# Performance work log

Hardware: AMD Instinct MI355X
Metric: run time of the kernel (lower is better)

## Reference

```python
import jax, jax.numpy as jnp
import numpy as np

EPS = 1e-4
SLOPE = 0.01
NFFT = 512
HOP = 256
CH_IN = 8
CH_H = 64
FREQ = NFFT // 2 + 1
LEN = 48000
BATCH = 2


def hann(n):
    return (0.5 - 0.5 * jnp.cos(2.0 * np.pi * jnp.arange(n) / n)).astype(jnp.float32)


def stft(x):
    # x: (B, C, L) -> (B, 2, C, F, T)  (torch.stft: center=True, reflect pad, hann window)
    pad = NFFT // 2
    xp = jnp.pad(x, ((0, 0), (0, 0), (pad, pad)), mode='reflect')
    T = 1 + x.shape[-1] // HOP
    idx = jnp.arange(T)[:, None] * HOP + jnp.arange(NFFT)[None, :]
    frames = xp[..., idx] * hann(NFFT)            # (B, C, T, NFFT)
    sp = jnp.fft.rfft(frames, axis=-1)            # (B, C, T, F)
    sp = jnp.swapaxes(sp, -1, -2)                 # (B, C, F, T)
    return jnp.stack([sp.real, sp.imag], axis=1).astype(jnp.float32)


def istft(re, im, length):
    # re, im: (B, C, F, T) -> (B, C, length) via windowed overlap-add
    sp = jnp.swapaxes(re + 1j * im, -1, -2)       # (B, C, T, F)
    win = hann(NFFT)
    frames = jnp.fft.irfft(sp, n=NFFT, axis=-1) * win
    pad = NFFT // 2
    total = length + 2 * pad
    T = frames.shape[-2]
    idx = jnp.arange(T)[:, None] * HOP + jnp.arange(NFFT)[None, :]
    out = jnp.zeros(frames.shape[:-2] + (total,), frames.dtype).at[..., idx].add(frames)
    wsum = jnp.zeros((total,), frames.dtype).at[idx].add(jnp.broadcast_to(win ** 2, (T, NFFT)))
    return (out / jnp.maximum(wsum, 1e-11))[..., pad:pad + length]


def conv2d(x, w, b, padT=0):
    y = jax.lax.conv_general_dilated(x, w, (1, 1), ((0, 0), (padT, padT)),
                                     dimension_numbers=('NCHW', 'OIHW', 'NCHW'))
    return y + b[None, :, None, None]


def cconv(x, w, b, padT=0):
    # complex conv on x: (B,2,C,F,T); w: (2,O,C,kf,kt) = [W_real, W_imag]; b: (2,O)
    r = conv2d(x[:, 0], w[0], b[0], padT) - conv2d(x[:, 1], w[1], b[1], padT)
    i = conv2d(x[:, 1], w[0], b[0], padT) + conv2d(x[:, 0], w[1], b[1], padT)
    return jnp.stack([r, i], axis=1)


def modExp(x, m=5.0):
    em = float(np.exp(m))
    return jnp.where(x > m, (x - m) * em + em, jnp.exp(jnp.minimum(x, m)))


def cExp(t):
    e = modExp(t[:, 0]) - 1.0
    return jnp.stack([e * jnp.cos(t[:, 1] - 1.0), e * jnp.sin(t[:, 1] - 1.0)], axis=1)


def snap(x):
    x = jnp.where((x >= 0) & (x < EPS), EPS, x)
    return jnp.where((x < 0) & (x > -EPS), -EPS, x)


def cLog(t):
    re = snap(t[:, 0])
    im = snap(t[:, 1])
    real = jnp.log(jnp.sqrt(im ** 2 + re ** 2 + EPS ** 2) + 1.0)
    imag = jnp.arctan(im / re)
    return jnp.stack([real, imag], axis=1)


def cMul(a, b):
    r = a[:, 0] * b[:, 0] - a[:, 1] * b[:, 1]
    i = a[:, 0] * b[:, 1] + a[:, 1] * b[:, 0]
    return jnp.stack([r, i], axis=1)


def trelu(t, tr, b):
    nr = t[:, 0] * tr[0, 0] + t[:, 1] * tr[0, 1] + b[0]
    ni = t[:, 0] * tr[1, 0] + t[:, 1] * tr[1, 1] + b[1]
    return jnp.stack([jax.nn.leaky_relu(nr, SLOPE), jax.nn.leaky_relu(ni, SLOPE)], axis=1)


def tgate(t, tr, b):
    gr = jax.nn.sigmoid(t[:, 0] * tr[0, 0] + t[:, 1] * tr[0, 1] + b[0])
    gi = jax.nn.sigmoid(t[:, 0] * tr[1, 0] + t[:, 1] * tr[1, 1] + b[1])
    return gr * gi + (1.0 - gr) * (1.0 - gi)


def perm(t):
    return jnp.transpose(t, (0, 1, 3, 2, 4))


def lrelu(x):
    return jax.nn.leaky_relu(x, SLOPE)


def forward(mix, fs_w, fs_b, fr_w, fr_b, c1r_w, c1r_b, c1i_w, c1i_b, c1_w, c1_b,
            c2r_w, c2r_b, c2i_w, c2i_b, c2_w, c2_b, a1_t, a1_b, a2_t, a2_b,
            c3r_w, c3r_b, c3i_w, c3i_b, c3_w, c3_b, c4r_w, c4r_b, c4i_w, c4i_b,
            c4_w, c4_b, a3_t, a3_b, a4_t, a4_b, f1_w, f1_b, f2_w, f2_b,
            cw_w, cw_b, fg_t, fg_b):
    ts = perm(cconv(perm(stft(mix)), fs_w, fs_b))      # (B,2,C,F,T)
    # ---- branch 1 ----
    tl = cLog(ts)
    tl = jnp.stack([conv2d(tl[:, 0], c1r_w, c1r_b), conv2d(tl[:, 1], c1r_w, c1r_b)], 1)
    tl = jnp.stack([conv2d(lrelu(tl[:, 0]), c1i_w, c1i_b), conv2d(tl[:, 1], c1i_w, c1i_b)], 1)
    tl = trelu(cExp(tl), a1_t, a1_b)
    t = cconv(tl, c1_w, c1_b)
    tl = cLog(t)
    tl = jnp.stack([conv2d(tl[:, 0], c2r_w, c2r_b, 7), conv2d(tl[:, 1], c2r_w, c2r_b, 7)], 1)[..., :-7]
    tl = jnp.stack([conv2d(lrelu(tl[:, 0]), c2i_w, c2i_b, 7), conv2d(tl[:, 1], c2i_w, c2i_b, 7)], 1)[..., :-7]
    tl = cExp(tl)
    tl1 = tl
    tc = cconv(ts, c2_w, c2_b, 7)[..., :-7]
    t = trelu(cMul(tl, tc), a2_t, a2_b)
    t = cconv(t, f1_w, f1_b)
    td1 = jnp.sum(ts - t, axis=2, keepdims=True) / ts.shape[2]
    # ---- branch 2 ----
    tl = cLog(ts)
    tl = jnp.stack([conv2d(tl[:, 0], c3r_w, c3r_b), conv2d(tl[:, 1], c3r_w, c3r_b)], 1)
    tl = jnp.stack([conv2d(lrelu(tl[:, 0]), c3i_w, c3i_b), conv2d(tl[:, 1], c3i_w, c3i_b)], 1)
    tl = trelu(cExp(tl), a3_t, a3_b)
    t = cconv(tl, c3_w, c3_b)
    tl = cLog(t)
    tl = jnp.stack([conv2d(tl[:, 0], c4r_w, c4r_b, 7), conv2d(tl[:, 1], c4r_w, c4r_b, 7)], 1)[..., :-7]
    tl = jnp.stack([conv2d(lrelu(tl[:, 0]), c4i_w, c4i_b, 7), conv2d(tl[:, 1], c4i_w, c4i_b, 7)], 1)[..., :-7]
    tl = cExp(tl)
    tc = cconv(ts, c4_w, c4_b, 7)[..., :-7]
    t = trelu(cMul(tl, tc), a4_t, a4_b)
    td2 = cconv(t, f2_w, f2_b)                         # (B,2,1,F,T)
    # ---- fuse ----
    f = cconv(jnp.concatenate([tl1, tl], axis=2), cw_w, cw_b)
    f = tgate(f, fg_t, fg_b)[:, None]                  # (B,1,1,F,T)
    td = td1 * f + td2 * (1.0 - f)
    t = perm(cconv(perm(td), fr_w, fr_b))
    return istft(t[:, 0], t[:, 1], LEN)                # (B,1,LEN)


def setup_inputs() -> dict:
    ks = iter(jax.random.split(jax.random.key(0), 64))
    def rn(shape, s=0.05):
        return s * jax.random.normal(next(ks), shape, jnp.float32)
    F, C, H = FREQ, CH_IN, CH_H
    inp = {
        'mix': jax.random.normal(next(ks), (BATCH, C, LEN), jnp.float32),
        'fs_w': rn((2, F, F, 1, 1)), 'fs_b': rn((2, F), 0.01),
        'fr_w': rn((2, F, F, 1, 1)), 'fr_b': rn((2, F), 0.01),
        'c1r_w': rn((H, C, 1, 1)), 'c1r_b': rn((H,), 0.01),
        'c1i_w': rn((H, H, 1, 1)), 'c1i_b': rn((H,), 0.01),
        'c1_w': rn((2, H, H, 1, 1)), 'c1_b': rn((2, H), 0.01),
        'c2r_w': rn((H, H, 1, 8)), 'c2r_b': rn((H,), 0.01),
        'c2i_w': rn((H, H, 1, 8)), 'c2i_b': rn((H,), 0.01),
        'c2_w': rn((2, H, C, 1, 8)), 'c2_b': rn((2, H), 0.01),
        'a1_t': rn((2, 2, H, F, 1), 0.5), 'a1_b': rn((2, H, F, 1), 0.5),
        'a2_t': rn((2, 2, H, F, 1), 0.5), 'a2_b': rn((2, H, F, 1), 0.5),
        'c3r_w': rn((H, C, 1, 1)), 'c3r_b': rn((H,), 0.01),
        'c3i_w': rn((H, H, 1, 1)), 'c3i_b': rn((H,), 0.01),
        'c3_w': rn((2, H, H, 1, 1)), 'c3_b': rn((2, H), 0.01),
        'c4r_w': rn((H, H, 1, 8)), 'c4r_b': rn((H,), 0.01),
        'c4i_w': rn((H, H, 1, 8)), 'c4i_b': rn((H,), 0.01),
        'c4_w': rn((2, H, C, 1, 8)), 'c4_b': rn((2, H), 0.01),
        'a3_t': rn((2, 2, H, F, 1), 0.5), 'a3_b': rn((2, H, F, 1), 0.5),
        'a4_t': rn((2, 2, H, F, 1), 0.5), 'a4_b': rn((2, H, F, 1), 0.5),
        'f1_w': rn((2, C, H, 1, 1)), 'f1_b': rn((2, C), 0.01),
        'f2_w': rn((2, 1, H, 1, 1)), 'f2_b': rn((2, 1), 0.01),
        'cw_w': rn((2, 1, 2 * H, 1, 1)), 'cw_b': rn((2, 1), 0.01),
        'fg_t': rn((2, 2, 1, F, 1), 0.5), 'fg_b': rn((2, 1, F, 1), 0.5),
    }
    return inp


def reference(mix, fs_w, fs_b, fr_w, fr_b, c1r_w, c1r_b, c1i_w, c1i_b, c1_w, c1_b,
              c2r_w, c2r_b, c2i_w, c2i_b, c2_w, c2_b, a1_t, a1_b, a2_t, a2_b,
              c3r_w, c3r_b, c3i_w, c3i_b, c3_w, c3_b, c4r_w, c4r_b, c4i_w, c4i_b,
              c4_w, c4_b, a3_t, a3_b, a4_t, a4_b, f1_w, f1_b, f2_w, f2_b,
              cw_w, cw_b, fg_t, fg_b):
    return forward(mix, fs_w, fs_b, fr_w, fr_b, c1r_w, c1r_b, c1i_w, c1i_b, c1_w, c1_b,
                   c2r_w, c2r_b, c2i_w, c2i_b, c2_w, c2_b, a1_t, a1_b, a2_t, a2_b,
                   c3r_w, c3r_b, c3i_w, c3i_b, c3_w, c3_b, c4r_w, c4r_b, c4i_w, c4i_b,
                   c4_w, c4_b, a3_t, a3_b, a4_t, a4_b, f1_w, f1_b, f2_w, f2_b,
                   cw_w, cw_b, fg_t, fg_b)
```

## Files before the change

kernel.cpp:

```cpp
#include <hip/hip_runtime.h>
#include <math.h>

#define DEV __device__ __forceinline__

constexpr int B_   = 2;
constexpr int C_IN = 8;
constexpr int H_   = 64;
constexpr int F_   = 257;
constexpr int T_   = 188;
constexpr int TW   = 96;
constexpr int NFFT = 512;
constexpr int HOP  = 256;
constexpr int LEN  = 48000;
constexpr int PADL = 256;
constexpr int FT   = F_ * T_;
constexpr float EPSV  = 1e-4f;
constexpr float SLOPEV = 0.01f;
constexpr float PI2 = 6.283185307179586f;

typedef __attribute__((ext_vector_type(8))) short short8;
typedef __attribute__((ext_vector_type(4))) short short4v;
typedef __attribute__((ext_vector_type(4))) float float4v;

DEV float lrelu_f(float x) { return x > 0.f ? x : SLOPEV * x; }
DEV float snap_f(float x) {
  if (x >= 0.f && x < EPSV) return EPSV;
  if (x < 0.f && x > -EPSV) return -EPSV;
  return x;
}
DEV float fast_atan(float z) {
  float az = fabsf(z);
  float u = az > 1.f ? __builtin_amdgcn_rcpf(az) : az;
  float u2 = u * u;
  float p = -0.01172120f;
  p = p * u2 + 0.05265332f;
  p = p * u2 - 0.11643287f;
  p = p * u2 + 0.19354346f;
  p = p * u2 - 0.33262347f;
  p = p * u2 + 0.99997726f;
  float r = p * u;
  if (az > 1.f) r = 1.5707963267948966f - r;
  return z < 0.f ? -r : r;
}
DEV float modexp_f(float x) {
  const float em = 148.4131591025766f;
  return x > 5.f ? (x - 5.f) * em + em : __expf(x);
}
DEV void cexp_f(float tr, float ti, float& er, float& ei) {
  float e = modexp_f(tr) - 1.f;
  float a = ti - 1.f;
  er = e * __cosf(a); ei = e * __sinf(a);
}
DEV float sigmoid_f(float x) { return 1.f / (1.f + __expf(-x)); }

DEV short f2bf(float x) {
  unsigned u = __float_as_uint(x);
  unsigned r = (u + 0x7fffu + ((u >> 16) & 1u)) >> 16;
  return (short)r;
}
DEV float bf2f(short h) {
  return __uint_as_float(((unsigned)(unsigned short)h) << 16);
}
DEV unsigned pack_hl(float v) {
  short hi = f2bf(v);
  short lo = f2bf(v - bf2f(hi));
  return ((unsigned)(unsigned short)hi << 16) | (unsigned)(unsigned short)lo;
}

__global__ void k_mixsplit(const float* __restrict__ x, short* __restrict__ hi,
                           short* __restrict__ lo) {
  int i = blockIdx.x * 256 + threadIdx.x;
  if (i >= B_ * C_IN * LEN / 4) return;
  float4v v = *(const float4v*)(x + (size_t)i * 4);
  short4v h, l;
  #pragma unroll
  for (int j = 0; j < 4; ++j) {
    h[j] = f2bf(v[j]);
    l[j] = f2bf(v[j] - bf2f(h[j]));
  }
  *(short4v*)(hi + (size_t)i * 4) = h;
  *(short4v*)(lo + (size_t)i * 4) = l;
}

__global__ __launch_bounds__(256) void k_mixdft(const float* __restrict__ W,
                                                short* __restrict__ wpk) {
  constexpr int MT = 33;
  __shared__ float wr_s[F_], wi_s[F_];
  int m = blockIdx.x;
  int k = blockIdx.y * 256 + threadIdx.x;
  int po = m >= F_;
  int fo = m - po * F_;
  if (m < 2 * F_) {
    for (int i = threadIdx.x; i < F_; i += 256) {
      wr_s[i] = W[fo * F_ + i];
      wi_s[i] = W[F_ * F_ + fo * F_ + i];
    }
  }
  __syncthreads();
  float val = 0.f;
  if (m < 2 * F_) {
    float sd, cd;
    sincosf((PI2 / NFFT) * k, &sd, &cd);
    float cs = 1.f, sn = 0.f;
    float ar = 0.f, ai = 0.f;
    for (int fi = 0; fi < F_; ++fi) {
      float wrv = wr_s[fi], wiv = wi_s[fi];
      ar += wrv * cs + wiv * sn;
      ai += wiv * cs - wrv * sn;
      float t2 = cs * cd - sn * sd;
      sn = sn * cd + cs * sd;
      cs = t2;
    }
    float win = 0.5f - 0.5f * cd;
    val = (po ? ai : ar) * win;
  }
  int mtg = m >> 4;
  int lane2 = ((k >> 3) & 3) * 16 + (m & 15);
  int s = k >> 5;
  int j = k & 7;
  short hi = f2bf(val);
  short lo = f2bf(val - bf2f(hi));
  wpk[(((0 * 16 + s) * MT + mtg) * 64 + lane2) * 8 + j] = hi;
  wpk[(((16 + s) * MT + mtg) * 64 + lane2) * 8 + j] = lo;
}

constexpr int TWS = 48;
__global__ __launch_bounds__(256) void k_stftmix(
    const short* __restrict__ mhi, const short* __restrict__ mlo,
    const short* __restrict__ wpk, const float* __restrict__ bias,
    float* __restrict__ Y) {
  constexpr int PITCH = 136;
  constexpr int MT = 33;
  __shared__ short xs_hi[TWS * PITCH];
  __shared__ short xs_lo[TWS * PITCH];
  int mg = blockIdx.x;
  int bc = blockIdx.y;
  int b = bc >> 3, c = bc & 7;
  int t0 = blockIdx.z * TWS;
  int tid = threadIdx.x;
  int lane = tid & 63;
  int wv = __builtin_amdgcn_readfirstlane(tid >> 6);
  int mtg = mg * 4 + wv;
  int q = lane >> 4;
  int n = lane & 15;

  const short* mh_ = mhi + (size_t)(b * C_IN + c) * LEN;
  const short* ml_ = mlo + (size_t)(b * C_IN + c) * LEN;

  float4v acc[3];
  #pragma unroll
  for (int nt = 0; nt < 3; ++nt) acc[nt] = (float4v)(0.f);

  const short8* wp = (const short8*)wpk;
  for (int round = 0; round < 4; ++round) {
    if (round) __syncthreads();
    for (int i = tid; i < TWS * 16; i += 256) {
      int tl = i >> 4, u = i & 15;
      int kk0 = u * 8;
      int t = t0 + tl;
      int g0 = t * HOP + round * 128 + kk0 - PADL;
      short8 h, l;
      if (t < T_ && g0 >= 0 && g0 + 7 < LEN) {
        h = *(const short8*)(mh_ + g0);
        l = *(const short8*)(ml_ + g0);
      } else {
        #pragma unroll
        for (int j = 0; j < 8; ++j) {
          short hv = 0, lv = 0;
          if (t < T_) {
            int g = g0 + j;
            if (g < 0) g = -g;
            if (g >= LEN) g = 2 * LEN - 2 - g;
            hv = mh_[g]; lv = ml_[g];
          }
          h[j] = hv; l[j] = lv;
        }
      }
      *(short8*)&xs_hi[tl * PITCH + kk0] = h;
      *(short8*)&xs_lo[tl * PITCH + kk0] = l;
    }
    __syncthreads();
    #pragma unroll
    for (int s2 = 0; s2 < 4; ++s2) {
      int s = round * 4 + s2;
      short8 Ah, Al;
      if (mtg < MT) {
        Ah = wp[((0 * 16 + s) * MT + mtg) * 64 + lane];
        Al = wp[((16 + s) * MT + mtg) * 64 + lane];
      }
      short8 Bh[3], Bl[3];
      #pragma unroll
      for (int nt = 0; nt < 3; ++nt) {
        int off = (nt * 16 + n) * PITCH + s2 * 32 + q * 8;
        Bh[nt] = *(const short8*)&xs_hi[off];
        Bl[nt] = *(const short8*)&xs_lo[off];
      }
      if (mtg < MT) {
        #pragma unroll
        for (int nt = 0; nt < 3; ++nt) {
          acc[nt] = __builtin_amdgcn_mfma_f32_16x16x32_bf16(Ah, Bh[nt], acc[nt], 0, 0, 0);
          acc[nt] = __builtin_amdgcn_mfma_f32_16x16x32_bf16(Ah, Bl[nt], acc[nt], 0, 0, 0);
          acc[nt] = __builtin_amdgcn_mfma_f32_16x16x32_bf16(Al, Bh[nt], acc[nt], 0, 0, 0);
        }
      }
    }
  }

  if (mtg < MT) {
    #pragma unroll
    for (int nt = 0; nt < 3; ++nt) {
      int t = t0 + nt * 16 + n;
      if (t >= T_) continue;
      #pragma unroll
      for (int r = 0; r < 4; ++r) {
        int m = mtg * 16 + q * 4 + r;
        if (m >= 2 * F_) continue;
        int po = m >= F_;
        int fo = m - po * F_;
        float badd = po ? bias[fo] + bias[F_ + fo] : bias[fo] - bias[F_ + fo];
        Y[((size_t)((b * 2 + po) * C_IN + c)) * FT + fo * T_ + t] = acc[nt][r] + badd;
      }
    }
  }
}

template<int CH>
__global__ void k_fmix(const float* __restrict__ X, const float* __restrict__ W,
                       const float* __restrict__ bias, float* __restrict__ Y) {
  int fo = blockIdx.x;
  int bc = blockIdx.y; int c = bc % CH; int b = bc / CH;
  int t = threadIdx.x;
  if (t >= T_) return;
  const float* wr = W + fo * F_;
  const float* wi = W + F_ * F_ + fo * F_;
  const float* xr = X + ((b * 2 + 0) * CH + c) * FT + t;
  const float* xi = X + ((b * 2 + 1) * CH + c) * FT + t;
  float ar = 0.f, ai = 0.f;
  for (int fi = 0; fi < F_; ++fi) {
    float wrv = wr[fi], wiv = wi[fi];
    float xrv = xr[fi * T_], xiv = xi[fi * T_];
    ar += wrv * xrv - wiv * xiv;
    ai += wrv * xiv + wiv * xrv;
  }
  float br = bias[fo], bi = bias[F_ + fo];
  Y[((b * 2 + 0) * CH + c) * FT + fo * T_ + t] = ar + br - bi;
  Y[((b * 2 + 1) * CH + c) * FT + fo * T_ + t] = ai + br + bi;
}

template<int CIN, int K>
DEV void repack_real_body(const float* __restrict__ W, short* __restrict__ wpk, int i) {
  constexpr int CC = (CIN >= 32) ? (CIN / 32) : 1;
  constexpr int NSTEP = (CIN * K + 31) / 32;
  int total = 2 * NSTEP * 4 * 64 * 8;
  if (i >= total) return;
  int j = i & 7;
  int lane = (i >> 3) & 63;
  int mt = (i >> 9) & 3;
  int s = (i >> 11) % NSTEP;
  int split = i / (NSTEP * 2048);
  int q = lane >> 4;
  int m = mt * 16 + (lane & 15);
  int tap = s / CC;
  int c = (s % CC) * 32 + q * 8 + j;
  float w = 0.f;
  if (c < CIN && tap < K) w = W[(m * CIN + c) * K + tap];
  short hi = f2bf(w);
  wpk[i] = split ? f2bf(w - bf2f(hi)) : hi;
}

template<int CIN2, int COUT2, int K>
DEV void repack_cplx_body(const float* __restrict__ W, short* __restrict__ wpk, int i) {
  constexpr int CIN = CIN2 / 2, COUT = COUT2 / 2;
  constexpr int NSTEP = CIN2 * K / 32;
  constexpr int MT = (COUT2 + 15) / 16;
  int total = 2 * NSTEP * MT * 64 * 8;
  if (i >= total) return;
  int j = i & 7;
  int lane = (i >> 3) & 63;
  int idx = i >> 9;
  int mt = idx % MT; idx /= MT;
  int s = idx % NSTEP;
  int split = idx / NSTEP;
  int q = lane >> 4;
  int m = mt * 16 + (lane & 15);
  int tap, pi, ci;
  if constexpr (CIN2 == 128) {
    tap = 0;
    int cs = s * 32 + q * 8 + j;
    int half = cs / 64, r = cs % 64;
    ci = half * 32 + r / 2;
    pi = r & 1;
  } else {
    tap = s * 2 + (q >> 1);
    int cs = (q & 1) * 8 + j;
    pi = cs / CIN;
    ci = cs % CIN;
  }
  float w = 0.f;
  if (m < COUT2) {
    int po = m / COUT, ho = m % COUT;
    float wr = W[((0 * COUT + ho) * CIN + ci) * K + tap];
    float wi = W[((1 * COUT + ho) * CIN + ci) * K + tap];
    w = (po == pi) ? wr : (po == 0 ? -wi : wi);
  }
  short hi = f2bf(w);
  wpk[i] = split ? f2bf(w - bf2f(hi)) : hi;
}

__global__ __launch_bounds__(256) void k_repack_all(
    const float* c1r_w, const float* c1i_w, const float* c2r_w, const float* c2i_w,
    const float* c3r_w, const float* c3i_w, const float* c4r_w, const float* c4i_w,
    const float* c1_w, const float* c2_w, const float* c3_w, const float* c4_w,
    const float* f1_w, const float* f2_w,
    short* o0, short* o1, short* o2, short* o3, short* o4, short* o5, short* o6,
    short* o7, short* o8, short* o9, short* o10, short* o11, short* o12, short* o13) {
  int i = blockIdx.x * 256 + threadIdx.x;
  switch (blockIdx.y) {
    case 0:  repack_real_body<C_IN, 1>(c1r_w, o0, i); break;
    case 1:  repack_real_body<H_,   1>(c1i_w, o1, i); break;
    case 2:  repack_real_body<H_,   8>(c2r_w, o2, i); break;
    case 3:  repack_real_body<H_,   8>(c2i_w, o3, i); break;
    case 4:  repack_real_body<C_IN, 1>(c3r_w, o4, i); break;
    case 5:  repack_real_body<H_,   1>(c3i_w, o5, i); break;
    case 6:  repack_real_body<H_,   8>(c4r_w, o6, i); break;
    case 7:  repack_real_body<H_,   8>(c4i_w, o7, i); break;
    case 8:  repack_cplx_body<128, 128, 1>(c1_w, o8, i); break;
    case 9:  repack_cplx_body<16,  128, 8>(c2_w, o9, i); break;
    case 10: repack_cplx_body<128, 128, 1>(c3_w, o10, i); break;
    case 11: repack_cplx_body<16,  128, 8>(c4_w, o11, i); break;
    case 12: repack_cplx_body<128, 16,  1>(f1_w, o12, i); break;
    case 13: repack_cplx_body<128, 2,   1>(f2_w, o13, i); break;
  }
}

template<int CIN, int K, int PRO, int EPI>
__global__ __launch_bounds__(256) void k_conv_mfma(
    const float* __restrict__ X, const short* __restrict__ wpk,
    const float* __restrict__ bias, float* __restrict__ Y) {
  constexpr int CC = (CIN >= 32) ? (CIN / 32) : 1;
  constexpr int NSTEP = (CIN * K + 31) / 32;
  constexpr int PITCH = 72;
  constexpr int ROWS = TW + (K - 1);
  __shared__ short xs_hi[ROWS * PITCH];
  __shared__ short xs_lo[ROWS * PITCH];
  int f = blockIdx.x;
  int bp = blockIdx.y; int p = bp & 1; int b = bp >> 1;
  int t0 = blockIdx.z * TW;
  int tid = threadIdx.x;

  {
    int lo_inval = (K - 1) - t0;
    if (lo_inval < 0) lo_inval = 0;
    int hi_start = T_ - t0 + (K - 1);
    if (hi_start > ROWS) hi_start = ROWS;
    for (int i = tid; i < lo_inval * PITCH; i += 256) { xs_hi[i] = 0; xs_lo[i] = 0; }
    int nhi = (ROWS - hi_start) * PITCH;
    for (int i = tid; i < nhi; i += 256) {
      int o = hi_start * PITCH + i;
      xs_hi[o] = 0; xs_lo[o] = 0;
    }
    if (CIN < 32) {
      constexpr int BAND = 32 - ((CIN < 32) ? CIN : 32);
      for (int i = tid; i < ROWS * BAND; i += 256) {
        int rr = i / BAND, c = CIN + i % BAND;
        xs_hi[rr * PITCH + c] = 0; xs_lo[rr * PITCH + c] = 0;
      }
    }
  }
  __syncthreads();

  const float* Xr_ = X + (size_t)((b * 2 + 0) * CIN) * FT + f * T_;
  const float* Xi_ = X + (size_t)((b * 2 + 1) * CIN) * FT + f * T_;
  const float* Xp  = X + (size_t)((b * 2 + p) * CIN) * FT + f * T_;
  const unsigned* Xu = (const unsigned*)X + (size_t)((b * 2 + p) * CIN) * FT + f * T_;
  {
    constexpr int STEP_C = 256 / ROWS, STEP_R = 256 % ROWS;
    int c = tid / ROWS;
    int rr = tid - c * ROWS;
    while (c < CIN) {
      int t = t0 + rr - (K - 1);
      if (t >= 0 && t < T_) {
        short hi, lo;
        if (PRO == 3) {
          unsigned v = Xu[c * FT + t];
          hi = (short)(v >> 16);
          lo = (short)(v & 0xffffu);
        } else {
          float v;
          if (PRO == 2) {
            float re = snap_f(Xr_[c * FT + t]);
            float im = snap_f(Xi_[c * FT + t]);
            v = (p == 0) ? __logf(sqrtf(im * im + re * re + EPSV * EPSV) + 1.f)
                         : fast_atan(im / re);
          } else {
            v = Xp[c * FT + t];
            if (PRO == 1 && p == 0) v = lrelu_f(v);
          }
          hi = f2bf(v);
          lo = f2bf(v - bf2f(hi));
        }
        xs_hi[rr * PITCH + c] = hi;
        xs_lo[rr * PITCH + c] = lo;
      }
      rr += STEP_R; c += STEP_C;
      if (rr >= ROWS) { rr -= ROWS; c += 1; }
    }
  }
  __syncthreads();

  int lane = tid & 63;
  int wv = __builtin_amdgcn_readfirstlane(tid >> 6);
  int mh = wv >> 1;
  int tc = wv & 1;
  int q = lane >> 4;
  int n = lane & 15;
  int wbase = tc * 48;

  float4v acc[2][3];
  #pragma unroll
  for (int mt = 0; mt < 2; ++mt)
    #pragma unroll
    for (int nt = 0; nt < 3; ++nt) acc[mt][nt] = (float4v)(0.f);

  const short8* wp = (const short8*)wpk;
  #pragma unroll
  for (int s = 0; s < NSTEP; ++s) {
    int tap = s / CC;
    int c0 = (s % CC) * 32;
    short8 Ah[2], Al[2];
    #pragma unroll
    for (int mt = 0; mt < 2; ++mt) {
      int mtg = mh * 2 + mt;
      Ah[mt] = wp[((0 * NSTEP + s) * 4 + mtg) * 64 + lane];
      Al[mt] = wp[((1 * NSTEP + s) * 4 + mtg) * 64 + lane];
    }
    short8 Bh[3], Bl[3];
    #pragma unroll
    for (int nt = 0; nt < 3; ++nt) {
      int off = (wbase + nt * 16 + n + tap) * PITCH + c0 + q * 8;
      Bh[nt] = *(const short8*)&xs_hi[off];
      Bl[nt] = *(const short8*)&xs_lo[off];
    }
    #pragma unroll
    for (int mt = 0; mt < 2; ++mt) {
      #pragma unroll
      for (int nt = 0; nt < 3; ++nt) {
        acc[mt][nt] = __builtin_amdgcn_mfma_f32_16x16x32_bf16(Ah[mt], Bh[nt], acc[mt][nt], 0, 0, 0);
        acc[mt][nt] = __builtin_amdgcn_mfma_f32_16x16x32_bf16(Ah[mt], Bl[nt], acc[mt][nt], 0, 0, 0);
        acc[mt][nt] = __builtin_amdgcn_mfma_f32_16x16x32_bf16(Al[mt], Bh[nt], acc[mt][nt], 0, 0, 0);
      }
    }
  }

  float* Yp = Y + (size_t)((b * 2 + p) * H_) * FT + f * T_;
  unsigned* Yu = (unsigned*)Y + (size_t)((b * 2 + p) * H_) * FT + f * T_;
  #pragma unroll
  for (int nt = 0; nt < 3; ++nt) {
    int t = t0 + wbase + nt * 16 + n;
    if (t >= T_) continue;
    #pragma unroll
    for (int mt = 0; mt < 2; ++mt) {
      #pragma unroll
      for (int r = 0; r < 4; ++r) {
        int h = (mh * 2 + mt) * 16 + q * 4 + r;
        float v = acc[mt][nt][r] + bias[h];
        if (EPI == 0) {
          Yp[h * FT + t] = v;
        } else {
          if (EPI == 1 && p == 0) v = lrelu_f(v);
          Yu[h * FT + t] = pack_hl(v);
        }
      }
    }
  }
}

template<int COUT2, int PRO>
__global__ __launch_bounds__(256) void k_cconv128(
    const float* __restrict__ X0, const float* __restrict__ X1,
    const short* __restrict__ wpk,
    const float* __restrict__ at, const float* __restrict__ ab,
    const float* __restrict__ bias, float* __restrict__ Y) {
  constexpr int MT = (COUT2 + 15) / 16;
  constexpr int MTW = (MT > 4) ? 4 : MT;
  constexpr int COUT = COUT2 / 2;
  constexpr int NSTEP = 4;
  constexpr int PITCH = 72;
  __shared__ short xs_hi[TW * PITCH];
  __shared__ short xs_lo[TW * PITCH];
  __shared__ float coef[6][64];
  int f = blockIdx.x;
  int b = blockIdx.y;
  int t0 = blockIdx.z * TW;
  int tid = threadIdx.x;
  int lane = tid & 63;
  int wv = __builtin_amdgcn_readfirstlane(tid >> 6);
  int mh = wv >> 1;
  int tc = wv & 1;
  int q = lane >> 4;
  int n = lane & 15;
  int wbase = tc * 48;

  if (tid < 64) {
    int h = tid;
    coef[0][h] = at[(0 * H_ + h) * F_ + f];
    coef[1][h] = at[(1 * H_ + h) * F_ + f];
    coef[2][h] = at[(2 * H_ + h) * F_ + f];
    coef[3][h] = at[(3 * H_ + h) * F_ + f];
    coef[4][h] = ab[h * F_ + f];
    coef[5][h] = ab[(H_ + h) * F_ + f];
  }
  {
    int inval0 = T_ - t0;
    if (inval0 < 0) inval0 = 0;
    if (inval0 > TW) inval0 = TW;
    int nfill = (TW - inval0) * PITCH;
    for (int i = tid; i < nfill; i += 256) {
      int o = inval0 * PITCH + i;
      xs_hi[o] = 0; xs_lo[o] = 0;
    }
  }

  const float* b0r = X0 + (size_t)((b * 2 + 0) * H_) * FT + f * T_;
  const float* b0i = X0 + (size_t)((b * 2 + 1) * H_) * FT + f * T_;
  const float* b1r = X1 + (size_t)((b * 2 + 0) * H_) * FT + f * T_;
  const float* b1i = X1 + (size_t)((b * 2 + 1) * H_) * FT + f * T_;

  float4v acc[MTW][3];
  #pragma unroll
  for (int mt = 0; mt < MTW; ++mt)
    #pragma unroll
    for (int nt = 0; nt < 3; ++nt) acc[mt][nt] = (float4v)(0.f);

  const short8* wp = (const short8*)wpk;
  for (int half = 0; half < 2; ++half) {
    __syncthreads();
    for (int i = tid; i < 32 * TW; i += 256) {
      int hh = i / TW, tl = i % TW;
      int t = t0 + tl;
      if (t >= T_) continue;
      int h = half * 32 + hh;
      float xr = b0r[h * FT + t], xi = b0i[h * FT + t];
      float vr, vi;
      if (PRO == 1) {
        float er, ei;
        cexp_f(xr, xi, er, ei);
        vr = lrelu_f(er * coef[0][h] + ei * coef[1][h] + coef[4][h]);
        vi = lrelu_f(er * coef[2][h] + ei * coef[3][h] + coef[5][h]);
      } else {
        float yr = b1r[h * FT + t], yi = b1i[h * FT + t];
        float mr = xr * yr - xi * yi;
        float mi = xr * yi + xi * yr;
        vr = lrelu_f(mr * coef[0][h] + mi * coef[1][h] + coef[4][h]);
        vi = lrelu_f(mr * coef[2][h] + mi * coef[3][h] + coef[5][h]);
      }
      int cs0 = hh * 2, cs1 = hh * 2 + 1;
      short hr = f2bf(vr), hi2 = f2bf(vi);
      xs_hi[tl * PITCH + cs0] = hr;
      xs_lo[tl * PITCH + cs0] = f2bf(vr - bf2f(hr));
      xs_hi[tl * PITCH + cs1] = hi2;
      xs_lo[tl * PITCH + cs1] = f2bf(vi - bf2f(hi2));
    }
    __syncthreads();
    #pragma unroll
    for (int s2 = 0; s2 < 2; ++s2) {
      int s = half * 2 + s2;
      short8 Bh[3], Bl[3];
      #pragma unroll
      for (int nt = 0; nt < 3; ++nt) {
        int off = (wbase + nt * 16 + n) * PITCH + s2 * 32 + q * 8;
        Bh[nt] = *(const short8*)&xs_hi[off];
        Bl[nt] = *(const short8*)&xs_lo[off];
      }
      #pragma unroll
      for (int mt = 0; mt < MTW; ++mt) {
        int mtg = mh * 4 + mt;
        if (mtg >= MT) continue;
        short8 Ah = wp[((0 * NSTEP + s) * MT + mtg) * 64 + lane];
        short8 Al = wp[((1 * NSTEP + s) * MT + mtg) * 64 + lane];
        #pragma unroll
        for (int nt = 0; nt < 3; ++nt) {
          acc[mt][nt] = __builtin_amdgcn_mfma_f32_16x16x32_bf16(Ah, Bh[nt], acc[mt][nt], 0, 0, 0);
          acc[mt][nt] = __builtin_amdgcn_mfma_f32_16x16x32_bf16(Ah, Bl[nt], acc[mt][nt], 0, 0, 0);
          acc[mt][nt] = __builtin_amdgcn_mfma_f32_16x16x32_bf16(Al, Bh[nt], acc[mt][nt], 0, 0, 0);
        }
      }
    }
  }

  float* Yp = Y + (size_t)b * COUT2 * FT + f * T_;
  #pragma unroll
  for (int nt = 0; nt < 3; ++nt) {
    int t = t0 + wbase + nt * 16 + n;
    if (t >= T_) continue;
    #pragma unroll
    for (int mt = 0; mt < MTW; ++mt) {
      int mtg = mh * 4 + mt;
      if (mtg >= MT) continue;
      #pragma unroll
      for (int r = 0; r < 4; ++r) {
        int o2 = mtg * 16 + q * 4 + r;
        if (o2 >= COUT2) continue;
        int po = o2 / COUT, ho = o2 % COUT;
        float br = bias[ho], bi = bias[COUT + ho];
        float badd = (po == 0) ? br - bi : br + bi;
        Yp[o2 * FT + t] = acc[mt][nt][r] + badd;
      }
    }
  }
}

__global__ __launch_bounds__(256) void k_cconv16(
    const float* __restrict__ X, const short* __restrict__ wpk,
    const float* __restrict__ bias, float* __restrict__ Y) {
  constexpr int MT = 8, NSTEP = 4, PITCH = 24, ROWS = TW + 7, COUT = 64, COUT2 = 128;
  __shared__ short xs_hi[ROWS * PITCH];
  __shared__ short xs_lo[ROWS * PITCH];
  int f = blockIdx.x;
  int b = blockIdx.y;
  int t0 = blockIdx.z * TW;
  int tid = threadIdx.x;

  {
    int lo_inval = 7 - t0;
    if (lo_inval < 0) lo_inval = 0;
    int hi_start = T_ - t0 + 7;
    if (hi_start > ROWS) hi_start = ROWS;
    for (int i = tid; i < lo_inval * PITCH; i += 256) { xs_hi[i] = 0; xs_lo[i] = 0; }
    int nhi = (ROWS - hi_start) * PITCH;
    for (int i = tid; i < nhi; i += 256) {
      int o = hi_start * PITCH + i;
      xs_hi[o] = 0; xs_lo[o] = 0;
    }
  }
  __syncthreads();

  const float* Xp = X + (size_t)b * 16 * FT + f * T_;
  for (int i = tid; i < 16 * ROWS; i += 256) {
    int c = i / ROWS, rr = i % ROWS;
    int t = t0 + rr - 7;
    if (t < 0 || t >= T_) continue;
    float v = Xp[c * FT + t];
    short hi = f2bf(v);
    short lo = f2bf(v - bf2f(hi));
    xs_hi[rr * PITCH + c] = hi;
    xs_lo[rr * PITCH + c] = lo;
  }
  __syncthreads();

  int lane = tid & 63;
  int wv = __builtin_amdgcn_readfirstlane(tid >> 6);
  int mh = wv >> 1;
  int tc = wv & 1;
  int q = lane >> 4;
  int n = lane & 15;
  int wbase = tc * 48;

  float4v acc[4][3];
  #pragma unroll
  for (int mt = 0; mt < 4; ++mt)
    #pragma unroll
    for (int nt = 0; nt < 3; ++nt) acc[mt][nt] = (float4v)(0.f);

  const short8* wp = (const short8*)wpk;
  #pragma unroll
  for (int s = 0; s < NSTEP; ++s) {
    int tap = s * 2 + (q >> 1);
    int coff = (q & 1) * 8;
    short8 Bh[3], Bl[3];
    #pragma unroll
    for (int nt = 0; nt < 3; ++nt) {
      int off = (wbase + nt * 16 + n + tap) * PITCH + coff;
      Bh[nt] = *(const short8*)&xs_hi[off];
      Bl[nt] = *(const short8*)&xs_lo[off];
    }
    #pragma unroll
    for (int mt = 0; mt < 4; ++mt) {
      int mtg = mh * 4 + mt;
      short8 Ah = wp[((0 * NSTEP + s) * MT + mtg) * 64 + lane];
      short8 Al = wp[((1 * NSTEP + s) * MT + mtg) * 64 + lane];
      #pragma unroll
      for (int nt = 0; nt < 3; ++nt) {
        acc[mt][nt] = __builtin_amdgcn_mfma_f32_16x16x32_bf16(Ah, Bh[nt], acc[mt][nt], 0, 0, 0);
        acc[mt][nt] = __builtin_amdgcn_mfma_f32_16x16x32_bf16(Ah, Bl[nt], acc[mt][nt], 0, 0, 0);
        acc[mt][nt] = __builtin_amdgcn_mfma_f32_16x16x32_bf16(Al, Bh[nt], acc[mt][nt], 0, 0, 0);
      }
    }
  }

  float* Yp = Y + (size_t)b * COUT2 * FT + f * T_;
  #pragma unroll
  for (int nt = 0; nt < 3; ++nt) {
    int t = t0 + wbase + nt * 16 + n;
    if (t >= T_) continue;
    #pragma unroll
    for (int mt = 0; mt < 4; ++mt) {
      #pragma unroll
      for (int r = 0; r < 4; ++r) {
        int o2 = (mh * 4 + mt) * 16 + q * 4 + r;
        int po = o2 / COUT, ho = o2 % COUT;
        float br = bias[ho], bi = bias[COUT + ho];
        float badd = (po == 0) ? br - bi : br + bi;
        Yp[o2 * FT + t] = acc[mt][nt][r] + badd;
      }
    }
  }
}

__global__ void k_cexp_pk(const unsigned* __restrict__ X, float* __restrict__ Y) {
  int i = blockIdx.x * blockDim.x + threadIdx.x;
  if (i >= B_ * H_ * FT) return;
  int b = i / (H_ * FT);
  int r = i % (H_ * FT);
  size_t i0 = (size_t)(b * 2) * H_ * FT + r;
  size_t i1 = i0 + (size_t)H_ * FT;
  unsigned v0 = X[i0], v1 = X[i1];
  float tr = bf2f((short)(v0 >> 16)) + bf2f((short)(v0 & 0xffffu));
  float ti = bf2f((short)(v1 >> 16)) + bf2f((short)(v1 & 0xffffu));
  float er, ei;
  cexp_f(tr, ti, er, ei);
  Y[i0] = er;
  Y[i1] = ei;
}

__global__ void k_td1(const float* __restrict__ ts, const float* __restrict__ t8,
                      float* __restrict__ td1) {
  int i = blockIdx.x * blockDim.x + threadIdx.x;
  if (i >= B_ * 2 * FT) return;
  int bp = i / FT; int r = i % FT;
  const float* a = ts + bp * C_IN * FT + r;
  const float* c2 = t8 + bp * C_IN * FT + r;
  float acc = 0.f;
  #pragma unroll
  for (int c = 0; c < C_IN; ++c) acc += a[c * FT] - c2[c * FT];
  td1[i] = acc * (1.f / C_IN);
}

__global__ void k_fuse(const float* __restrict__ tl1, const float* __restrict__ tl2,
                       const float* __restrict__ td1, const float* __restrict__ td2,
                       const float* __restrict__ cw, const float* __restrict__ cwb,
                       const float* __restrict__ fgt, const float* __restrict__ fgb,
                       float* __restrict__ td) {
  int i = blockIdx.x * blockDim.x + threadIdx.x;
  if (i >= B_ * FT) return;
  int b = i / FT; int r = i % FT; int f = r / T_;
  const float* x1r = tl1 + (b * 2) * H_ * FT + r;
  const float* x1i = x1r + H_ * FT;
  const float* x2r = tl2 + (b * 2) * H_ * FT + r;
  const float* x2i = x2r + H_ * FT;
  float fr = 0.f, fi = 0.f;
  for (int c = 0; c < H_; ++c) {
    float w1r = cw[c], w2r = cw[H_ + c], w1i = cw[2 * H_ + c], w2i = cw[3 * H_ + c];
    float a1r = x1r[c * FT], a1i = x1i[c * FT];
    float a2r = x2r[c * FT], a2i = x2i[c * FT];
    fr += w1r * a1r - w1i * a1i + w2r * a2r - w2i * a2i;
    fi += w1r * a1i + w1i * a1r + w2r * a2i + w2i * a2r;
  }
  fr += cwb[0] - cwb[1];
  fi += cwb[0] + cwb[1];
  float t00 = fgt[f], t01 = fgt[F_ + f], t10 = fgt[2 * F_ + f], t11 = fgt[3 * F_ + f];
  float gr = sigmoid_f(fr * t00 + fi * t01 + fgb[f]);
  float gi = sigmoid_f(fr * t10 + fi * t11 + fgb[F_ + f]);
  float gg = gr * gi + (1.f - gr) * (1.f - gi);
  int i0 = (b * 2) * FT + r, i1 = i0 + FT;
  td[i0] = td1[i0] * gg + td2[i0] * (1.f - gg);
  td[i1] = td1[i1] * gg + td2[i1] * (1.f - gg);
}

__global__ __launch_bounds__(320) void k_iframes(const float* __restrict__ sp,
                                                 float* __restrict__ frames) {
  __shared__ float Xr[F_], Xi[F_];
  int blk = blockIdx.x;
  int t = blk % T_;
  int b = blk / T_;
  int tid = threadIdx.x;
  for (int i = tid; i < F_; i += 320) {
    Xr[i] = sp[(b * 2 + 0) * FT + i * T_ + t];
    Xi[i] = sp[(b * 2 + 1) * FT + i * T_ + t];
  }
  __syncthreads();
  int n = tid;
  if (n <= 256) {
    float sd, cd;
    sincosf((PI2 / NFFT) * n, &sd, &cd);
    float cs = cd, sn = sd;
    float ac = 0.f, as = 0.f;
    for (int f = 1; f < 256; ++f) {
      ac += Xr[f] * cs;
      as += Xi[f] * sn;
      float t2 = cs * cd - sn * sd;
      sn = sn * cd + cs * sd;
      cs = t2;
    }
    float base = Xr[0] + Xr[256] * (1.f - 2.f * (n & 1));
    float win = 0.5f - 0.5f * cd;
    float scale = win * (1.f / NFFT);
    float* fr = frames + (size_t)(b * T_ + t) * NFFT;
    fr[n] = (base + 2.f * ac - 2.f * as) * scale;
    if (n >= 1 && n <= 255)
      fr[NFFT - n] = (base + 2.f * ac + 2.f * as) * scale;
  }
}

__global__ void k_ola(const float* __restrict__ frames, float* __restrict__ out) {
  int i = blockIdx.x * blockDim.x + threadIdx.x;
  if (i >= B_ * LEN) return;
  int b = i / LEN; int j = i % LEN;
  int p = j + PADL;
  int t0 = p / HOP; int n0 = p - t0 * HOP;
  float acc = 0.f, wsum = 0.f;
  if (t0 < T_) {
    acc += frames[(b * T_ + t0) * NFFT + n0];
    float w = 0.5f - 0.5f * __cosf((PI2 / NFFT) * n0);
    wsum += w * w;
  }
  int t1 = t0 - 1, n1 = n0 + HOP;
  if (t1 >= 0 && t1 < T_) {
    acc += frames[(b * T_ + t1) * NFFT + n1];
    float w = 0.5f - 0.5f * __cosf((PI2 / NFFT) * n1);
    wsum += w * w;
  }
  out[i] = acc / fmaxf(wsum, 1e-11f);
}

extern "C" void kernel_launch(void* const* d_in, const int* in_sizes, int n_in,
                              void* d_out, int out_size, void* d_ws, size_t ws_size,
                              hipStream_t stream) {
  const float* mix   = (const float*)d_in[0];
  const float* fs_w  = (const float*)d_in[1];
  const float* fs_b  = (const float*)d_in[2];
  const float* fr_w  = (const float*)d_in[3];
  const float* fr_b  = (const float*)d_in[4];
  const float* c1r_w = (const float*)d_in[5];
  const float* c1r_b = (const float*)d_in[6];
  const float* c1i_w = (const float*)d_in[7];
  const float* c1i_b = (const float*)d_in[8];
  const float* c1_w  = (const float*)d_in[9];
  const float* c1_b  = (const float*)d_in[10];
  const float* c2r_w = (const float*)d_in[11];
  const float* c2r_b = (const float*)d_in[12];
  const float* c2i_w = (const float*)d_in[13];
  const float* c2i_b = (const float*)d_in[14];
  const float* c2_w  = (const float*)d_in[15];
  const float* c2_b  = (const float*)d_in[16];
  const float* a1_t  = (const float*)d_in[17];
  const float* a1_b  = (const float*)d_in[18];
  const float* a2_t  = (const float*)d_in[19];
  const float* a2_b  = (const float*)d_in[20];
  const float* c3r_w = (const float*)d_in[21];
  const float* c3r_b = (const float*)d_in[22];
  const float* c3i_w = (const float*)d_in[23];
  const float* c3i_b = (const float*)d_in[24];
  const float* c3_w  = (const float*)d_in[25];
  const float* c3_b  = (const float*)d_in[26];
  const float* c4r_w = (const float*)d_in[27];
  const float* c4r_b = (const float*)d_in[28];
  const float* c4i_w = (const float*)d_in[29];
  const float* c4i_b = (const float*)d_in[30];
  const float* c4_w  = (const float*)d_in[31];
  const float* c4_b  = (const float*)d_in[32];
  const float* a3_t  = (const float*)d_in[33];
  const float* a3_b  = (const float*)d_in[34];
  const float* a4_t  = (const float*)d_in[35];
  const float* a4_b  = (const float*)d_in[36];
  const float* f1_w  = (const float*)d_in[37];
  const float* f1_b  = (const float*)d_in[38];
  const float* f2_w  = (const float*)d_in[39];
  const float* f2_b  = (const float*)d_in[40];
  const float* cw_w  = (const float*)d_in[41];
  const float* cw_b  = (const float*)d_in[42];
  const float* fg_t  = (const float*)d_in[43];
  const float* fg_b  = (const float*)d_in[44];

  const size_t S8 = (size_t)B_ * 2 * C_IN * FT;
  const size_t SH = (size_t)B_ * 2 * H_ * FT;
  const size_t S1 = (size_t)B_ * 2 * FT;
  float* ws  = (float*)d_ws;
  float* ts0 = ws;
  float* ts  = ts0 + S8;
  float* A   = ts + S8;
  float* Bb  = A + SH;
  float* Cc  = Bb + SH;
  float* td1 = Cc + SH;
  float* td2 = td1 + S1;
  float* tdf = td2 + S1;
  float* tdr = tdf + S1;
  float* s8  = ts0;
  float* frames = ts0;

  short* wtail = (short*)(tdr + S1);
  constexpr int SZ_C8K1   = 2 * 1  * 4 * 64 * 8;
  constexpr int SZ_C64K1  = 2 * 2  * 4 * 64 * 8;
  constexpr int SZ_C64K8  = 2 * 16 * 4 * 64 * 8;
  constexpr int SZ_CC128  = 2 * 4  * 8 * 64 * 8;
  constexpr int SZ_CF     = 2 * 4  * 1 * 64 * 8;
  constexpr int SZ_SM     = 2 * 16 * 33 * 64 * 8;
  short* w_c1r = wtail;
  short* w_c1i = w_c1r + SZ_C8K1;
  short* w_c2r = w_c1i + SZ_C64K1;
  short* w_c2i = w_c2r + SZ_C64K8;
  short* w_c3r = w_c2i + SZ_C64K8;
  short* w_c3i = w_c3r + SZ_C8K1;
  short* w_c4r = w_c3i + SZ_C64K1;
  short* w_c4i = w_c4r + SZ_C64K8;
  short* w_cc1 = w_c4i + SZ_C64K8;
  short* w_cc2 = w_cc1 + SZ_CC128;
  short* w_cc3 = w_cc2 + SZ_CC128;
  short* w_cc4 = w_cc3 + SZ_CC128;
  short* w_cf1 = w_cc4 + SZ_CC128;
  short* w_cf2 = w_cf1 + SZ_CF;
  short* w_sm  = w_cf2 + SZ_CF;
  short* mhi   = w_sm + SZ_SM;
  short* mlo   = mhi + (size_t)B_ * C_IN * LEN;

  const int nH = B_ * H_ * FT;
  const int nP = B_ * FT;
  const dim3 rgrid(F_, B_ * 2, 2);
  const dim3 cgrid(F_, B_, 2);

  k_repack_all<<<dim3(256, 14), 256, 0, stream>>>(
      c1r_w, c1i_w, c2r_w, c2i_w, c3r_w, c3i_w, c4r_w, c4i_w,
      c1_w, c2_w, c3_w, c4_w, f1_w, f2_w,
      w_c1r, w_c1i, w_c2r, w_c2i, w_c3r, w_c3i, w_c4r, w_c4i,
      w_cc1, w_cc2, w_cc3, w_cc4, w_cf1, w_cf2);

  k_mixsplit<<<(B_ * C_IN * LEN / 4 + 255) / 256, 256, 0, stream>>>(mix, mhi, mlo);
  k_mixdft<<<dim3(528, 2), 256, 0, stream>>>(fs_w, w_sm);
  k_stftmix<<<dim3(9, 16, 4), 256, 0, stream>>>(mhi, mlo, w_sm, fs_b, ts);

  k_conv_mfma<C_IN, 1, 2, 1><<<rgrid, 256, 0, stream>>>(ts, w_c1r, c1r_b, A);
  k_conv_mfma<H_, 1, 3, 0><<<rgrid, 256, 0, stream>>>(A, w_c1i, c1i_b, Bb);
  k_cconv128<128, 1><<<cgrid, 256, 0, stream>>>(Bb, Bb, w_cc1, a1_t, a1_b, c1_b, A);
  k_conv_mfma<H_, 8, 2, 1><<<rgrid, 256, 0, stream>>>(A, w_c2r, c2r_b, Bb);
  k_conv_mfma<H_, 8, 3, 2><<<rgrid, 256, 0, stream>>>(Bb, w_c2i, c2i_b, A);
  k_cexp_pk<<<(nH + 255) / 256, 256, 0, stream>>>((const unsigned*)A, Bb);
  k_cconv16<<<cgrid, 256, 0, stream>>>(ts, w_cc2, c2_b, A);
  k_cconv128<16, 2><<<cgrid, 256, 0, stream>>>(Bb, A, w_cf1, a2_t, a2_b, f1_b, s8);
  k_td1<<<(B_ * 2 * FT + 255) / 256, 256, 0, stream>>>(ts, s8, td1);

  k_conv_mfma<C_IN, 1, 2, 1><<<rgrid, 256, 0, stream>>>(ts, w_c3r, c3r_b, A);
  k_conv_mfma<H_, 1, 3, 0><<<rgrid, 256, 0, stream>>>(A, w_c3i, c3i_b, Cc);
  k_cconv128<128, 1><<<cgrid, 256, 0, stream>>>(Cc, Cc, w_cc3, a3_t, a3_b, c3_b, A);
  k_conv_mfma<H_, 8, 2, 1><<<rgrid, 256, 0, stream>>>(A, w_c4r, c4r_b, Cc);
  k_conv_mfma<H_, 8, 3, 2><<<rgrid, 256, 0, stream>>>(Cc, w_c4i, c4i_b, A);
  k_cexp_pk<<<(nH + 255) / 256, 256, 0, stream>>>((const unsigned*)A, Cc);
  k_cconv16<<<cgrid, 256, 0, stream>>>(ts, w_cc4, c4_b, A);
  k_cconv128<2, 2><<<cgrid, 256, 0, stream>>>(Cc, A, w_cf2, a4_t, a4_b, f2_b, td2);

  k_fuse<<<(nP + 255) / 256, 256, 0, stream>>>(Bb, Cc, td1, td2, cw_w, cw_b, fg_t, fg_b, tdf);
  k_fmix<1><<<dim3(F_, B_), 192, 0, stream>>>(tdf, fr_w, fr_b, tdr);
  k_iframes<<<B_ * T_, 320, 0, stream>>>(tdr, frames);
  k_ola<<<(B_ * LEN + 255) / 256, 256, 0, stream>>>(frames, (float*)d_out);
}
```

Before: 815.4 us.

## Batch the two independent conv branches into shared launches

```diff
diff --git a/kernel.cpp b/kernel.cpp
--- a/kernel.cpp
+++ b/kernel.cpp
@@ -335,8 +335,10 @@
 
 template<int CIN, int K, int PRO, int EPI>
 __global__ __launch_bounds__(256) void k_conv_mfma(
-    const float* __restrict__ X, const short* __restrict__ wpk,
-    const float* __restrict__ bias, float* __restrict__ Y) {
+    const float* __restrict__ Xa, const float* __restrict__ Xb,
+    const short* __restrict__ wpka, const short* __restrict__ wpkb,
+    const float* __restrict__ biasa, const float* __restrict__ biasb,
+    float* __restrict__ Ya, float* __restrict__ Yb) {
   constexpr int CC = (CIN >= 32) ? (CIN / 32) : 1;
   constexpr int NSTEP = (CIN * K + 31) / 32;
   constexpr int PITCH = 72;
@@ -344,7 +346,14 @@
   __shared__ short xs_hi[ROWS * PITCH];
   __shared__ short xs_lo[ROWS * PITCH];
   int f = blockIdx.x;
-  int bp = blockIdx.y; int p = bp & 1; int b = bp >> 1;
+  int y = blockIdx.y;
+  int brsel = (y >= B_ * 2);
+  int bp = y - brsel * (B_ * 2);
+  int p = bp & 1; int b = bp >> 1;
+  const float* X = brsel ? Xb : Xa;
+  const short* wpk = brsel ? wpkb : wpka;
+  const float* bias = brsel ? biasb : biasa;
+  float* Y = brsel ? Yb : Ya;
   int t0 = blockIdx.z * TW;
   int tid = threadIdx.x;
 
@@ -477,10 +486,13 @@
 
 template<int COUT2, int PRO>
 __global__ __launch_bounds__(256) void k_cconv128(
-    const float* __restrict__ X0, const float* __restrict__ X1,
-    const short* __restrict__ wpk,
-    const float* __restrict__ at, const float* __restrict__ ab,
-    const float* __restrict__ bias, float* __restrict__ Y) {
+    const float* __restrict__ X0a, const float* __restrict__ X1a,
+    const float* __restrict__ X0b, const float* __restrict__ X1b,
+    const short* __restrict__ wpka, const short* __restrict__ wpkb,
+    const float* __restrict__ ata, const float* __restrict__ atb,
+    const float* __restrict__ aba, const float* __restrict__ abb,
+    const float* __restrict__ biasa, const float* __restrict__ biasb,
+    float* __restrict__ Ya, float* __restrict__ Yb) {
   constexpr int MT = (COUT2 + 15) / 16;
   constexpr int MTW = (MT > 4) ? 4 : MT;
   constexpr int COUT = COUT2 / 2;
@@ -490,7 +502,16 @@
   __shared__ short xs_lo[TW * PITCH];
   __shared__ float coef[6][64];
   int f = blockIdx.x;
-  int b = blockIdx.y;
+  int y = blockIdx.y;
+  int brsel = (y >= B_);
+  int b = y - brsel * B_;
+  const float* X0 = brsel ? X0b : X0a;
+  const float* X1 = brsel ? X1b : X1a;
+  const short* wpk = brsel ? wpkb : wpka;
+  const float* at = brsel ? atb : ata;
+  const float* ab = brsel ? abb : aba;
+  const float* bias = brsel ? biasb : biasa;
+  float* Y = brsel ? Yb : Ya;
   int t0 = blockIdx.z * TW;
   int tid = threadIdx.x;
   int lane = tid & 63;
@@ -602,8 +623,8 @@
         int o2 = mtg * 16 + q * 4 + r;
         if (o2 >= COUT2) continue;
         int po = o2 / COUT, ho = o2 % COUT;
-        float br = bias[ho], bi = bias[COUT + ho];
-        float badd = (po == 0) ? br - bi : br + bi;
+        float br2 = bias[ho], bi2 = bias[COUT + ho];
+        float badd = (po == 0) ? br2 - bi2 : br2 + bi2;
         Yp[o2 * FT + t] = acc[mt][nt][r] + badd;
       }
     }
@@ -611,13 +632,21 @@
 }
 
 __global__ __launch_bounds__(256) void k_cconv16(
-    const float* __restrict__ X, const short* __restrict__ wpk,
-    const float* __restrict__ bias, float* __restrict__ Y) {
+    const float* __restrict__ Xa, const float* __restrict__ Xb,
+    const short* __restrict__ wpka, const short* __restrict__ wpkb,
+    const float* __restrict__ biasa, const float* __restrict__ biasb,
+    float* __restrict__ Ya, float* __restrict__ Yb) {
   constexpr int MT = 8, NSTEP = 4, PITCH = 24, ROWS = TW + 7, COUT = 64, COUT2 = 128;
   __shared__ short xs_hi[ROWS * PITCH];
   __shared__ short xs_lo[ROWS * PITCH];
   int f = blockIdx.x;
-  int b = blockIdx.y;
+  int y = blockIdx.y;
+  int brsel = (y >= B_);
+  int b = y - brsel * B_;
+  const float* X = brsel ? Xb : Xa;
+  const short* wpk = brsel ? wpkb : wpka;
+  const float* bias = brsel ? biasb : biasa;
+  float* Y = brsel ? Yb : Ya;
   int t0 = blockIdx.z * TW;
   int tid = threadIdx.x;
 
@@ -699,19 +728,24 @@
       for (int r = 0; r < 4; ++r) {
         int o2 = (mh * 4 + mt) * 16 + q * 4 + r;
         int po = o2 / COUT, ho = o2 % COUT;
-        float br = bias[ho], bi = bias[COUT + ho];
-        float badd = (po == 0) ? br - bi : br + bi;
+        float br2 = bias[ho], bi2 = bias[COUT + ho];
+        float badd = (po == 0) ? br2 - bi2 : br2 + bi2;
         Yp[o2 * FT + t] = acc[mt][nt][r] + badd;
       }
     }
   }
 }
 
-__global__ void k_cexp_pk(const unsigned* __restrict__ X, float* __restrict__ Y) {
+__global__ void k_cexp_pk(const unsigned* __restrict__ Xa, const unsigned* __restrict__ Xb,
+                          float* __restrict__ Ya, float* __restrict__ Yb) {
   int i = blockIdx.x * blockDim.x + threadIdx.x;
-  if (i >= B_ * H_ * FT) return;
-  int b = i / (H_ * FT);
-  int r = i % (H_ * FT);
+  if (i >= 2 * B_ * H_ * FT) return;
+  int brsel = (i >= B_ * H_ * FT);
+  int j = i - brsel * (B_ * H_ * FT);
+  const unsigned* X = brsel ? Xb : Xa;
+  float* Y = brsel ? Yb : Ya;
+  int b = j / (H_ * FT);
+  int r = j % (H_ * FT);
   size_t i0 = (size_t)(b * 2) * H_ * FT + r;
   size_t i1 = i0 + (size_t)H_ * FT;
   unsigned v0 = X[i0], v1 = X[i1];
@@ -878,8 +912,9 @@
   float* ws  = (float*)d_ws;
   float* ts0 = ws;
   float* ts  = ts0 + S8;
-  float* A   = ts + S8;
-  float* Bb  = A + SH;
+  float* A1  = ts + S8;
+  float* A2  = A1 + SH;
+  float* Bb  = A2 + SH;
   float* Cc  = Bb + SH;
   float* td1 = Cc + SH;
   float* td2 = td1 + S1;
@@ -915,7 +950,8 @@
 
   const int nH = B_ * H_ * FT;
   const int nP = B_ * FT;
-  const dim3 rgrid(F_, B_ * 2, 2);
+  const dim3 mrgrid(F_, 2 * B_ * 2, 2);
+  const dim3 mcgrid(F_, 2 * B_, 2);
   const dim3 cgrid(F_, B_, 2);
 
   k_repack_all<<<dim3(256, 14), 256, 0, stream>>>(
@@ -928,24 +964,28 @@
   k_mixdft<<<dim3(528, 2), 256, 0, stream>>>(fs_w, w_sm);
   k_stftmix<<<dim3(9, 16, 4), 256, 0, stream>>>(mhi, mlo, w_sm, fs_b, ts);
 
-  k_conv_mfma<C_IN, 1, 2, 1><<<rgrid, 256, 0, stream>>>(ts, w_c1r, c1r_b, A);
-  k_conv_mfma<H_, 1, 3, 0><<<rgrid, 256, 0, stream>>>(A, w_c1i, c1i_b, Bb);
-  k_cconv128<128, 1><<<cgrid, 256, 0, stream>>>(Bb, Bb, w_cc1, a1_t, a1_b, c1_b, A);
-  k_conv_mfma<H_, 8, 2, 1><<<rgrid, 256, 0, stream>>>(A, w_c2r, c2r_b, Bb);
-  k_conv_mfma<H_, 8, 3, 2><<<rgrid, 256, 0, stream>>>(Bb, w_c2i, c2i_b, A);
-  k_cexp_pk<<<(nH + 255) / 256, 256, 0, stream>>>((const unsigned*)A, Bb);
-  k_cconv16<<<cgrid, 256, 0, stream>>>(ts, w_cc2, c2_b, A);
-  k_cconv128<16, 2><<<cgrid, 256, 0, stream>>>(Bb, A, w_cf1, a2_t, a2_b, f1_b, s8);
+  k_conv_mfma<C_IN, 1, 2, 1><<<mrgrid, 256, 0, stream>>>(
+      ts, ts, w_c1r, w_c3r, c1r_b, c3r_b, A1, A2);
+  k_conv_mfma<H_, 1, 3, 0><<<mrgrid, 256, 0, stream>>>(
+      A1, A2, w_c1i, w_c3i, c1i_b, c3i_b, Bb, Cc);
+  k_cconv128<128, 1><<<mcgrid, 256, 0, stream>>>(
+      Bb, Bb, Cc, Cc, w_cc1, w_cc3, a1_t, a3_t, a1_b, a3_b,
+      c1_b, c3_b, A1, A2);
+  k_conv_mfma<H_, 8, 2, 1><<<mrgrid, 256, 0, stream>>>(
+      A1, A2, w_c2r, w_c4r, c2r_b, c4r_b, Bb, Cc);
+  k_conv_mfma<H_, 8, 3, 2><<<mrgrid, 256, 0, stream>>>(
+      Bb, Cc, w_c2i, w_c4i, c2i_b, c4i_b, A1, A2);
+  k_cexp_pk<<<(2 * nH + 255) / 256, 256, 0, stream>>>(
+      (const unsigned*)A1, (const unsigned*)A2, Bb, Cc);
+  k_cconv16<<<mcgrid, 256, 0, stream>>>(
+      ts, ts, w_cc2, w_cc4, c2_b, c4_b, A1, A2);
+  k_cconv128<16, 2><<<cgrid, 256, 0, stream>>>(
+      Bb, A1, Bb, A1, w_cf1, w_cf1, a2_t, a2_t, a2_b, a2_b,
+      f1_b, f1_b, s8, s8);
   k_td1<<<(B_ * 2 * FT + 255) / 256, 256, 0, stream>>>(ts, s8, td1);
-
-  k_conv_mfma<C_IN, 1, 2, 1><<<rgrid, 256, 0, stream>>>(ts, w_c3r, c3r_b, A);
-  k_conv_mfma<H_, 1, 3, 0><<<rgrid, 256, 0, stream>>>(A, w_c3i, c3i_b, Cc);
-  k_cconv128<128, 1><<<cgrid, 256, 0, stream>>>(Cc, Cc, w_cc3, a3_t, a3_b, c3_b, A);
-  k_conv_mfma<H_, 8, 2, 1><<<rgrid, 256, 0, stream>>>(A, w_c4r, c4r_b, Cc);
-  k_conv_mfma<H_, 8, 3, 2><<<rgrid, 256, 0, stream>>>(Cc, w_c4i, c4i_b, A);
-  k_cexp_pk<<<(nH + 255) / 256, 256, 0, stream>>>((const unsigned*)A, Cc);
-  k_cconv16<<<cgrid, 256, 0, stream>>>(ts, w_cc4, c4_b, A);
-  k_cconv128<2, 2><<<cgrid, 256, 0, stream>>>(Cc, A, w_cf2, a4_t, a4_b, f2_b, td2);
+  k_cconv128<2, 2><<<cgrid, 256, 0, stream>>>(
+      Cc, A2, Cc, A2, w_cf2, w_cf2, a4_t, a4_t, a4_b, a4_b,
+      f2_b, f2_b, td2, td2);
 
   k_fuse<<<(nP + 255) / 256, 256, 0, stream>>>(Bb, Cc, td1, td2, cw_w, cw_b, fg_t, fg_b, tdf);
   k_fmix<1><<<dim3(F_, B_), 192, 0, stream>>>(tdf, fr_w, fr_b, tdr);
```

Measured after the change: 771.2 us. 5.4% less time.
